# Kernel tuning notes

Measured on AMD Instinct MI355X. Metric: run time of the kernel, lower is better.

Reference implementation:

```python
import jax, jax.numpy as jnp
import numpy as np

N = 100000
E = 1600000
IN_C = 256
HID = 256
OUT_C = 32
K = 2          # APPNP K = max(1, num_layers)
ALPHA = 0.1


def setup_inputs() -> dict:
    key = jax.random.key(0)
    ks = jax.random.split(key, 8)
    x = jax.random.normal(ks[0], (N, IN_C), dtype=jnp.float32)
    edge_index = jax.random.randint(ks[1], (2, E), 0, N, dtype=jnp.int64)
    s_in = 1.0 / np.sqrt(IN_C)
    s_h = 1.0 / np.sqrt(HID)
    W_in = jax.random.uniform(ks[2], (IN_C, HID), jnp.float32, -s_in, s_in)
    b_in = jax.random.uniform(ks[3], (HID,), jnp.float32, -s_in, s_in)
    W_h = jax.random.uniform(ks[4], (HID, HID), jnp.float32, -s_h, s_h)
    b_h = jax.random.uniform(ks[5], (HID,), jnp.float32, -s_h, s_h)
    W_out = jax.random.uniform(ks[6], (HID, OUT_C), jnp.float32, -s_h, s_h)
    b_out = jax.random.uniform(ks[7], (OUT_C,), jnp.float32, -s_h, s_h)
    return {"x": x, "edge_index": edge_index, "W_in": W_in, "b_in": b_in,
            "W_h": W_h, "b_h": b_h, "W_out": W_out, "b_out": b_out}


def _appnp(h0, src, dst):
    # gcn_norm with added self-loops: deg over destinations, sym normalization
    loops = jnp.arange(N, dtype=src.dtype)
    src_f = jnp.concatenate([src, loops])  # [E+N]
    dst_f = jnp.concatenate([dst, loops])
    deg = jax.ops.segment_sum(jnp.ones_like(dst_f, dtype=h0.dtype), dst_f,
                              num_segments=N)
    dinv = jnp.where(deg > 0, jax.lax.rsqrt(jnp.maximum(deg, 1e-12)), 0.0)
    norm = (dinv[src_f] * dinv[dst_f])[:, None]  # [E+N, 1]
    h = h0
    for _ in range(K):
        agg = jax.ops.segment_sum(h[src_f] * norm, dst_f, num_segments=N)
        h = (1.0 - ALPHA) * agg + ALPHA * h0
    return h


def reference(x, edge_index, W_in, b_in, W_h, b_h, W_out, b_out):
    # MLP encoder (dropout inactive in eval mode)
    h = jax.nn.relu(x @ W_in + b_in)
    h = jax.nn.relu(h @ W_h + b_h)
    h = h @ W_out + b_out  # [N, OUT_C]
    return _appnp(h, edge_index[0], edge_index[1])
```

## Files before the change

kernel.cpp:

```cpp
#include <hip/hip_runtime.h>

#define NN 100000
#define NE 1600000
#define NT64 1563

#define BSH 7
#define BNODES 128
#define NBUCK 782
#define NBUCKP 784
#define CAP 2560
#define ECH 8192
#define NCHK 196
#define WFRAG_BLKS 272

typedef _Float16 half8v __attribute__((ext_vector_type(8)));
typedef _Float16 half4v __attribute__((ext_vector_type(4)));
typedef float f32x4 __attribute__((ext_vector_type(4)));


__device__ __forceinline__ void wfrag_one(const float* __restrict__ W,
                                          _Float16* __restrict__ Wf, int idx, int N) {
    int j = idx & 7;
    int l = (idx >> 3) & 63;
    int f = idx >> 9;
    int nt = f % (N / 16);
    int kt = f / (N / 16);
    int k = kt * 32 + (l >> 4) * 8 + j;
    int c = nt * 16 + (l & 15);
    Wf[idx] = (_Float16)W[k * N + c];
}


__global__ __launch_bounds__(512) void k_count_wfrag(const int* __restrict__ dst,
                                                     int* __restrict__ histT,
                                                     const float* __restrict__ W1,
                                                     const float* __restrict__ W2,
                                                     const float* __restrict__ W3,
                                                     _Float16* __restrict__ Wf1,
                                                     _Float16* __restrict__ Wf2,
                                                     _Float16* __restrict__ Wf3) {
    const int t = threadIdx.x;
    if (blockIdx.x >= NCHK) {
        int idx = (blockIdx.x - NCHK) * 512 + t;
        if (idx < 65536) wfrag_one(W1, Wf1, idx, 256);
        else if (idx < 131072) wfrag_one(W2, Wf2, idx - 65536, 256);
        else if (idx < 139264) wfrag_one(W3, Wf3, idx - 131072, 32);
        return;
    }
    __shared__ int h[NBUCKP];
    const int blk = blockIdx.x;
    for (int b = t; b < NBUCKP; b += 512) h[b] = 0;
    __syncthreads();
    const int ebase = blk * ECH + t * 16;
#pragma unroll
    for (int q = 0; q < 4; q++) {
        int e = ebase + q * 4;
        if (e + 4 <= NE) {
            int4 d4 = *reinterpret_cast<const int4*>(dst + e);
            atomicAdd(&h[d4.x >> BSH], 1);
            atomicAdd(&h[d4.y >> BSH], 1);
            atomicAdd(&h[d4.z >> BSH], 1);
            atomicAdd(&h[d4.w >> BSH], 1);
        } else {
            for (int p = e; p < NE; p++) atomicAdd(&h[dst[p] >> BSH], 1);
            break;
        }
    }
    __syncthreads();
    for (int b = t; b < NBUCK; b += 512) histT[(long long)b * NCHK + blk] = h[b];
}


__global__ __launch_bounds__(256) void k_scanb(int* __restrict__ histT,
                                               int* __restrict__ cntb) {
    __shared__ int s[256];
    const int b = blockIdx.x, t = threadIdx.x;
    int* row = histT + (long long)b * NCHK;
    int v = (t < NCHK) ? row[t] : 0;
    s[t] = v;
    __syncthreads();
    for (int off = 1; off < 256; off <<= 1) {
        int u = (t >= off) ? s[t - off] : 0;
        __syncthreads();
        s[t] += u;
        __syncthreads();
    }
    if (t < NCHK) row[t] = s[t] - v;
    if (t == 255) cntb[b] = s[255];
}


__global__ __launch_bounds__(512) void k_part(const int* __restrict__ src,
                                              const int* __restrict__ dst,
                                              const int* __restrict__ histT,
                                              int* __restrict__ data) {
    __shared__ int curs[NBUCKP];
    const int t = threadIdx.x, blk = blockIdx.x;
    for (int b = t; b < NBUCKP; b += 512)
        curs[b] = b * CAP + ((b < NBUCK) ? histT[(long long)b * NCHK + blk] : 0);
    __syncthreads();
    const int ebase = blk * ECH + t * 16;
#pragma unroll
    for (int q = 0; q < 4; q++) {
        int e = ebase + q * 4;
        if (e + 4 <= NE) {
            int4 d4 = *reinterpret_cast<const int4*>(dst + e);
            int4 s4 = *reinterpret_cast<const int4*>(src + e);
            int p0 = atomicAdd(&curs[d4.x >> BSH], 1);
            data[p0] = (s4.x << BSH) | (d4.x & (BNODES - 1));
            int p1 = atomicAdd(&curs[d4.y >> BSH], 1);
            data[p1] = (s4.y << BSH) | (d4.y & (BNODES - 1));
            int p2 = atomicAdd(&curs[d4.z >> BSH], 1);
            data[p2] = (s4.z << BSH) | (d4.z & (BNODES - 1));
            int p3 = atomicAdd(&curs[d4.w >> BSH], 1);
            data[p3] = (s4.w << BSH) | (d4.w & (BNODES - 1));
        } else {
            for (int p = e; p < NE; p++) {
                int d = dst[p], sv = src[p];
                int pos = atomicAdd(&curs[d >> BSH], 1);
                data[pos] = (sv << BSH) | (d & (BNODES - 1));
            }
            break;
        }
    }
}


__global__ __launch_bounds__(256) void k_sortb(const int* __restrict__ data,
                                               const int* __restrict__ cntb,
                                               int* __restrict__ col,
                                               int* __restrict__ begp,
                                               int* __restrict__ endp,
                                               float* __restrict__ dinv) {
    __shared__ int hist[BNODES];
    __shared__ int scn[BNODES];
    __shared__ int curs[BNODES];
    const int b = blockIdx.x, t = threadIdx.x;
    if (t < BNODES) hist[t] = 0;
    __syncthreads();
    const int cnt = cntb[b];
    const int* wp = data + b * CAP;
    for (int e = t; e < cnt; e += 256) atomicAdd(&hist[wp[e] & (BNODES - 1)], 1);
    __syncthreads();
    if (t < BNODES) scn[t] = hist[t];
    __syncthreads();
    for (int off = 1; off < BNODES; off <<= 1) {
        int v = (t < BNODES && t >= off) ? scn[t - off] : 0;
        __syncthreads();
        if (t < BNODES) scn[t] += v;
        __syncthreads();
    }
    if (t < BNODES) {
        int beg = scn[t] - hist[t];
        curs[t] = beg;
        int node = (b << BSH) + t;
        if (node < NN) {
            begp[node] = b * CAP + beg;
            endp[node] = b * CAP + scn[t];
            dinv[node] = rsqrtf((float)(hist[t] + 1));
        }
    }
    __syncthreads();
    for (int e = t; e < cnt; e += 256) {
        int w = wp[e];
        int p = atomicAdd(&curs[w & (BNODES - 1)], 1);
        col[b * CAP + p] = w >> BSH;
    }
}


__global__ __launch_bounds__(512) void k_mlp(const float* __restrict__ x,
                                             const _Float16* __restrict__ Wf1,
                                             const _Float16* __restrict__ Wf2,
                                             const _Float16* __restrict__ Wf3,
                                             const float* __restrict__ b1,
                                             const float* __restrict__ b2,
                                             const float* __restrict__ b3,
                                             const float* __restrict__ dinv,
                                             _Float16* __restrict__ h0f,
                                             _Float16* __restrict__ hs0) {
    __shared__ char buf[64 * 512];
    const int t = threadIdx.x;
    const int lane = t & 63;
    const int G = lane >> 4;
    const int w = t >> 6;
    const int T = blockIdx.x;
    const long long row0 = (long long)T * 64;

    const half8v* W1f = reinterpret_cast<const half8v*>(Wf1);
    const half8v* W2f = reinterpret_cast<const half8v*>(Wf2);
    float bv1[2], bv2[2];
#pragma unroll
    for (int n2 = 0; n2 < 2; n2++) {
        bv1[n2] = b1[w * 32 + n2 * 16 + (lane & 15)];
        bv2[n2] = b2[w * 32 + n2 * 16 + (lane & 15)];
    }

    {
        const float4* A4 = reinterpret_cast<const float4*>(x + row0 * 256);
        float4 v[8];
#pragma unroll
        for (int q = 0; q < 8; q++) {
            int i = t + q * 512;
            int r = i >> 6;
            v[q] = make_float4(0.f, 0.f, 0.f, 0.f);
            if (row0 + r < NN) v[q] = A4[i];
        }
        __builtin_amdgcn_sched_barrier(0);
#pragma unroll
        for (int q = 0; q < 8; q++) {
            int i = t + q * 512;
            int r = i >> 6, c4 = i & 63;
            half4v hv;
            hv[0] = (_Float16)v[q].x; hv[1] = (_Float16)v[q].y;
            hv[2] = (_Float16)v[q].z; hv[3] = (_Float16)v[q].w;
            int bo = (r * 512 + c4 * 8) ^ ((r & 7) << 4);
            *reinterpret_cast<half4v*>(buf + bo) = hv;
        }
    }
    __syncthreads();

    f32x4 acc[4][2];

#pragma unroll
    for (int mt = 0; mt < 4; mt++)
#pragma unroll
        for (int n2 = 0; n2 < 2; n2++) acc[mt][n2] = (f32x4)0.f;
#pragma unroll
    for (int kt = 0; kt < 8; kt++) {
        half8v a[4], bfr[2];
#pragma unroll
        for (int n2 = 0; n2 < 2; n2++)
            bfr[n2] = W1f[(kt * 16 + 2 * w + n2) * 64 + lane];
#pragma unroll
        for (int mt = 0; mt < 4; mt++) {
            int row = mt * 16 + (lane & 15);
            int bo = (row * 512 + kt * 64 + (G << 4)) ^ ((row & 7) << 4);
            a[mt] = *reinterpret_cast<const half8v*>(buf + bo);
        }
#pragma unroll
        for (int mt = 0; mt < 4; mt++)
#pragma unroll
            for (int n2 = 0; n2 < 2; n2++)
                acc[mt][n2] = __builtin_amdgcn_mfma_f32_16x16x32_f16(a[mt], bfr[n2], acc[mt][n2], 0, 0, 0);
    }
    __syncthreads();

#pragma unroll
    for (int mt = 0; mt < 4; mt++)
#pragma unroll
        for (int n2 = 0; n2 < 2; n2++) {
            int colc = w * 32 + n2 * 16 + (lane & 15);
            float bb = bv1[n2];
#pragma unroll
            for (int r = 0; r < 4; r++) {
                int row = mt * 16 + G * 4 + r;
                float v = fmaxf(acc[mt][n2][r] + bb, 0.f);
                int bo = (row * 512 + colc * 2) ^ ((row & 7) << 4);
                *reinterpret_cast<_Float16*>(buf + bo) = (_Float16)v;
            }
        }
    __syncthreads();

#pragma unroll
    for (int mt = 0; mt < 4; mt++)
#pragma unroll
        for (int n2 = 0; n2 < 2; n2++) acc[mt][n2] = (f32x4)0.f;
#pragma unroll
    for (int kt = 0; kt < 8; kt++) {
        half8v a[4], bfr[2];
#pragma unroll
        for (int n2 = 0; n2 < 2; n2++)
            bfr[n2] = W2f[(kt * 16 + 2 * w + n2) * 64 + lane];
#pragma unroll
        for (int mt = 0; mt < 4; mt++) {
            int row = mt * 16 + (lane & 15);
            int bo = (row * 512 + kt * 64 + (G << 4)) ^ ((row & 7) << 4);
            a[mt] = *reinterpret_cast<const half8v*>(buf + bo);
        }
#pragma unroll
        for (int mt = 0; mt < 4; mt++)
#pragma unroll
            for (int n2 = 0; n2 < 2; n2++)
                acc[mt][n2] = __builtin_amdgcn_mfma_f32_16x16x32_f16(a[mt], bfr[n2], acc[mt][n2], 0, 0, 0);
    }
    __syncthreads();

#pragma unroll
    for (int mt = 0; mt < 4; mt++)
#pragma unroll
        for (int n2 = 0; n2 < 2; n2++) {
            int colc = w * 32 + n2 * 16 + (lane & 15);
            float bb = bv2[n2];
#pragma unroll
            for (int r = 0; r < 4; r++) {
                int row = mt * 16 + G * 4 + r;
                float v = fmaxf(acc[mt][n2][r] + bb, 0.f);
                int bo = (row * 512 + colc * 2) ^ ((row & 7) << 4);
                *reinterpret_cast<_Float16*>(buf + bo) = (_Float16)v;
            }
        }
    __syncthreads();

    {
        const half8v* W3f = reinterpret_cast<const half8v*>(Wf3);
        const int mt3 = w >> 1, ct3 = w & 1;
        const float bb3 = b3[ct3 * 16 + (lane & 15)];
        f32x4 a3 = (f32x4)0.f;
#pragma unroll
        for (int kt = 0; kt < 8; kt++) {
            int row = mt3 * 16 + (lane & 15);
            int bo = (row * 512 + kt * 64 + (G << 4)) ^ ((row & 7) << 4);
            half8v a = *reinterpret_cast<const half8v*>(buf + bo);
            half8v b = W3f[(kt * 2 + ct3) * 64 + lane];
            a3 = __builtin_amdgcn_mfma_f32_16x16x32_f16(a, b, a3, 0, 0, 0);
        }
        int colc = ct3 * 16 + (lane & 15);
#pragma unroll
        for (int r = 0; r < 4; r++) {
            long long row = row0 + mt3 * 16 + G * 4 + r;
            if (row < NN) {
                float v = a3[r] + bb3;
                h0f[row * 32 + colc] = (_Float16)v;
                hs0[row * 32 + colc] = (_Float16)(dinv[row] * v);
            }
        }
    }
}


template<bool FINAL>
__global__ __launch_bounds__(256) void k_appnp(const int* __restrict__ begp,
                                               const int* __restrict__ endp,
                                               const int* __restrict__ col,
                                               const float* __restrict__ dinv,
                                               const _Float16* __restrict__ hs,
                                               const _Float16* __restrict__ h0f,
                                               void* __restrict__ outp) {
    int node = blockIdx.x * 4 + (threadIdx.x >> 6);
    if (node >= NN) return;
    const int lane = threadIdx.x & 63;
    const int slot = lane >> 2;
    const int cg = lane & 3;

    const int beg = begp[node];
    const int end = endp[node];
    const float dd = dinv[node];
    const half8v selfv = *reinterpret_cast<const half8v*>(hs + (size_t)node * 32 + cg * 8);
    const half8v h0v = *reinterpret_cast<const half8v*>(h0f + (size_t)node * 32 + cg * 8);

    float acc[8];
#pragma unroll
    for (int j = 0; j < 8; j++) acc[j] = 0.f;

    for (int e = beg + slot; e < end; e += 16) {
        int s = col[e];
        half8v v = *reinterpret_cast<const half8v*>(hs + (size_t)s * 32 + cg * 8);
#pragma unroll
        for (int j = 0; j < 8; j++) acc[j] += (float)v[j];
    }

#pragma unroll
    for (int off = 4; off < 64; off <<= 1) {
#pragma unroll
        for (int j = 0; j < 8; j++) acc[j] += __shfl_xor(acc[j], off, 64);
    }

    if (slot == 0) {
        float o[8];
#pragma unroll
        for (int j = 0; j < 8; j++)
            o[j] = 0.9f * dd * (acc[j] + (float)selfv[j]) + 0.1f * (float)h0v[j];
        size_t off = (size_t)node * 32 + cg * 8;
        if (FINAL) {
            float4 v0 = make_float4(o[0], o[1], o[2], o[3]);
            float4 v1 = make_float4(o[4], o[5], o[6], o[7]);
            float4* op = reinterpret_cast<float4*>((float*)outp + off);
            op[0] = v0; op[1] = v1;
        } else {
            half8v hv;
#pragma unroll
            for (int j = 0; j < 8; j++) hv[j] = (_Float16)(dd * o[j]);
            *reinterpret_cast<half8v*>((_Float16*)outp + off) = hv;
        }
    }
}


extern "C" void kernel_launch(void* const* d_in, const int* in_sizes, int n_in,
                              void* d_out, int out_size, void* d_ws, size_t ws_size,
                              hipStream_t stream) {
    const float* x     = (const float*)d_in[0];
    const int*   ei    = (const int*)d_in[1];
    const float* W_in  = (const float*)d_in[2];
    const float* b_in  = (const float*)d_in[3];
    const float* W_h   = (const float*)d_in[4];
    const float* b_h   = (const float*)d_in[5];
    const float* W_out = (const float*)d_in[6];
    const float* b_out = (const float*)d_in[7];
    float* out = (float*)d_out;

    const int* srcv = ei;
    const int* dstv = ei + NE;

    char* ws = (char*)d_ws;
    _Float16* h0f  = (_Float16*)ws;
    _Float16* hs0  = h0f + (size_t)NN * 32;
    _Float16* hs1  = hs0 + (size_t)NN * 32;
    float* dinv    = (float*)(hs1 + (size_t)NN * 32);
    _Float16* Wf_in  = (_Float16*)(dinv + NN);
    _Float16* Wf_h   = Wf_in + 256 * 256;
    _Float16* Wf_out = Wf_h + 256 * 256;
    int* histT = (int*)(Wf_out + 256 * 32);
    int* cntb  = histT + (size_t)NBUCK * NCHK;
    int* data  = cntb + NBUCKP;
    int* col   = data + (size_t)NBUCKP * CAP;
    int* begp  = col + (size_t)NBUCKP * CAP;
    int* endp  = begp + NN;

    k_count_wfrag<<<NCHK + WFRAG_BLKS, 512, 0, stream>>>(dstv, histT,
                                                         W_in, W_h, W_out,
                                                         Wf_in, Wf_h, Wf_out);
    k_scanb<<<NBUCK, 256, 0, stream>>>(histT, cntb);

    k_part<<<NCHK, 512, 0, stream>>>(srcv, dstv, histT, data);

    k_sortb<<<NBUCK, 256, 0, stream>>>(data, cntb, col, begp, endp, dinv);

    k_mlp<<<NT64, 512, 0, stream>>>(x, Wf_in, Wf_h, Wf_out, b_in, b_h, b_out,
                                    dinv, h0f, hs0);

    k_appnp<false><<<(NN + 3) / 4, 256, 0, stream>>>(begp, endp, col, dinv, hs0, h0f, hs1);
    k_appnp<true ><<<(NN + 3) / 4, 256, 0, stream>>>(begp, endp, col, dinv, hs1, h0f, out);
}
```

Before: 170.8 us.

## Merge edge partition with MLP launch and defer dinv scaling to sort kernel

Removes the MLP's dependence on dinv so the edge partition blocks and the MLP blocks can share one launch and run concurrently. Degree computation moves to a small separate kernel, and the dinv-scaled copy hs0 is now produced by extra blocks appended to the bucket sort kernel. The goal is to hide the latency-bound partition and sort phases behind the compute-heavy MLP. The cost is one additional launch (k_deg), a second pass over the bucketed data to count degrees, and an extra read and write of h0f to build hs0.

```diff
diff --git a/kernel.cpp b/kernel.cpp
--- a/kernel.cpp
+++ b/kernel.cpp
@@ -3,6 +3,7 @@
 #define NN 100000
 #define NE 1600000
 #define NT64 1563
+#define SCALE_BLKS 1563
 
 #define BSH 7
 #define BNODES 128
@@ -90,101 +91,59 @@
 }
 
 
-__global__ __launch_bounds__(512) void k_part(const int* __restrict__ src,
-                                              const int* __restrict__ dst,
-                                              const int* __restrict__ histT,
-                                              int* __restrict__ data) {
-    __shared__ int curs[NBUCKP];
-    const int t = threadIdx.x, blk = blockIdx.x;
-    for (int b = t; b < NBUCKP; b += 512)
-        curs[b] = b * CAP + ((b < NBUCK) ? histT[(long long)b * NCHK + blk] : 0);
-    __syncthreads();
-    const int ebase = blk * ECH + t * 16;
-#pragma unroll
-    for (int q = 0; q < 4; q++) {
-        int e = ebase + q * 4;
-        if (e + 4 <= NE) {
-            int4 d4 = *reinterpret_cast<const int4*>(dst + e);
-            int4 s4 = *reinterpret_cast<const int4*>(src + e);
-            int p0 = atomicAdd(&curs[d4.x >> BSH], 1);
-            data[p0] = (s4.x << BSH) | (d4.x & (BNODES - 1));
-            int p1 = atomicAdd(&curs[d4.y >> BSH], 1);
-            data[p1] = (s4.y << BSH) | (d4.y & (BNODES - 1));
-            int p2 = atomicAdd(&curs[d4.z >> BSH], 1);
-            data[p2] = (s4.z << BSH) | (d4.z & (BNODES - 1));
-            int p3 = atomicAdd(&curs[d4.w >> BSH], 1);
-            data[p3] = (s4.w << BSH) | (d4.w & (BNODES - 1));
-        } else {
-            for (int p = e; p < NE; p++) {
-                int d = dst[p], sv = src[p];
-                int pos = atomicAdd(&curs[d >> BSH], 1);
-                data[pos] = (sv << BSH) | (d & (BNODES - 1));
+__global__ __launch_bounds__(512) void k_part_mlp(const int* __restrict__ src,
+                                                  const int* __restrict__ dst,
+                                                  const int* __restrict__ histT,
+                                                  int* __restrict__ data,
+                                                  const float* __restrict__ x,
+                                                  const _Float16* __restrict__ Wf1,
+                                                  const _Float16* __restrict__ Wf2,
+                                                  const _Float16* __restrict__ Wf3,
+                                                  const float* __restrict__ b1,
+                                                  const float* __restrict__ b2,
+                                                  const float* __restrict__ b3,
+                                                  _Float16* __restrict__ h0f) {
+    __shared__ char smem[32768];
+    const int t = threadIdx.x;
+
+    if (blockIdx.x < NCHK) {
+        int* curs = (int*)smem;
+        const int blk = blockIdx.x;
+        for (int b = t; b < NBUCKP; b += 512)
+            curs[b] = b * CAP + ((b < NBUCK) ? histT[(long long)b * NCHK + blk] : 0);
+        __syncthreads();
+        const int ebase = blk * ECH + t * 16;
+#pragma unroll
+        for (int q = 0; q < 4; q++) {
+            int e = ebase + q * 4;
+            if (e + 4 <= NE) {
+                int4 d4 = *reinterpret_cast<const int4*>(dst + e);
+                int4 s4 = *reinterpret_cast<const int4*>(src + e);
+                int p0 = atomicAdd(&curs[d4.x >> BSH], 1);
+                data[p0] = (s4.x << BSH) | (d4.x & (BNODES - 1));
+                int p1 = atomicAdd(&curs[d4.y >> BSH], 1);
+                data[p1] = (s4.y << BSH) | (d4.y & (BNODES - 1));
+                int p2 = atomicAdd(&curs[d4.z >> BSH], 1);
+                data[p2] = (s4.z << BSH) | (d4.z & (BNODES - 1));
+                int p3 = atomicAdd(&curs[d4.w >> BSH], 1);
+                data[p3] = (s4.w << BSH) | (d4.w & (BNODES - 1));
+            } else {
+                for (int p = e; p < NE; p++) {
+                    int d = dst[p], sv = src[p];
+                    int pos = atomicAdd(&curs[d >> BSH], 1);
+                    data[pos] = (sv << BSH) | (d & (BNODES - 1));
+                }
+                break;
             }
-            break;
-        }
-    }
-}
-
-
-__global__ __launch_bounds__(256) void k_sortb(const int* __restrict__ data,
-                                               const int* __restrict__ cntb,
-                                               int* __restrict__ col,
-                                               int* __restrict__ begp,
-                                               int* __restrict__ endp,
-                                               float* __restrict__ dinv) {
-    __shared__ int hist[BNODES];
-    __shared__ int scn[BNODES];
-    __shared__ int curs[BNODES];
-    const int b = blockIdx.x, t = threadIdx.x;
-    if (t < BNODES) hist[t] = 0;
-    __syncthreads();
-    const int cnt = cntb[b];
-    const int* wp = data + b * CAP;
-    for (int e = t; e < cnt; e += 256) atomicAdd(&hist[wp[e] & (BNODES - 1)], 1);
-    __syncthreads();
-    if (t < BNODES) scn[t] = hist[t];
-    __syncthreads();
-    for (int off = 1; off < BNODES; off <<= 1) {
-        int v = (t < BNODES && t >= off) ? scn[t - off] : 0;
-        __syncthreads();
-        if (t < BNODES) scn[t] += v;
-        __syncthreads();
-    }
-    if (t < BNODES) {
-        int beg = scn[t] - hist[t];
-        curs[t] = beg;
-        int node = (b << BSH) + t;
-        if (node < NN) {
-            begp[node] = b * CAP + beg;
-            endp[node] = b * CAP + scn[t];
-            dinv[node] = rsqrtf((float)(hist[t] + 1));
-        }
-    }
-    __syncthreads();
-    for (int e = t; e < cnt; e += 256) {
-        int w = wp[e];
-        int p = atomicAdd(&curs[w & (BNODES - 1)], 1);
-        col[b * CAP + p] = w >> BSH;
-    }
-}
-
-
-__global__ __launch_bounds__(512) void k_mlp(const float* __restrict__ x,
-                                             const _Float16* __restrict__ Wf1,
-                                             const _Float16* __restrict__ Wf2,
-                                             const _Float16* __restrict__ Wf3,
-                                             const float* __restrict__ b1,
-                                             const float* __restrict__ b2,
-                                             const float* __restrict__ b3,
-                                             const float* __restrict__ dinv,
-                                             _Float16* __restrict__ h0f,
-                                             _Float16* __restrict__ hs0) {
-    __shared__ char buf[64 * 512];
-    const int t = threadIdx.x;
+        }
+        return;
+    }
+
+    char* buf = smem;
     const int lane = t & 63;
     const int G = lane >> 4;
     const int w = t >> 6;
-    const int T = blockIdx.x;
+    const int T = blockIdx.x - NCHK;
     const long long row0 = (long long)T * 64;
 
     const half8v* W1f = reinterpret_cast<const half8v*>(Wf1);
@@ -319,12 +278,82 @@
 #pragma unroll
         for (int r = 0; r < 4; r++) {
             long long row = row0 + mt3 * 16 + G * 4 + r;
-            if (row < NN) {
-                float v = a3[r] + bb3;
-                h0f[row * 32 + colc] = (_Float16)v;
-                hs0[row * 32 + colc] = (_Float16)(dinv[row] * v);
-            }
-        }
+            if (row < NN) h0f[row * 32 + colc] = (_Float16)(a3[r] + bb3);
+        }
+    }
+}
+
+
+__global__ __launch_bounds__(256) void k_deg(const int* __restrict__ data,
+                                             const int* __restrict__ cntb,
+                                             float* __restrict__ dinv) {
+    __shared__ int c[BNODES];
+    const int b = blockIdx.x, t = threadIdx.x;
+    if (t < BNODES) c[t] = 0;
+    __syncthreads();
+    const int cnt = cntb[b];
+    const int* wp = data + b * CAP;
+    for (int e = t; e < cnt; e += 256) atomicAdd(&c[wp[e] & (BNODES - 1)], 1);
+    __syncthreads();
+    int node = (b << BSH) + t;
+    if (t < BNODES && node < NN) dinv[node] = rsqrtf((float)(c[t] + 1));
+}
+
+
+__global__ __launch_bounds__(256) void k_sortb_scale(const int* __restrict__ data,
+                                                     const int* __restrict__ cntb,
+                                                     int* __restrict__ col,
+                                                     int* __restrict__ begp,
+                                                     int* __restrict__ endp,
+                                                     const float* __restrict__ dinv,
+                                                     const _Float16* __restrict__ h0f,
+                                                     _Float16* __restrict__ hs0) {
+    const int t = threadIdx.x;
+    if (blockIdx.x >= NBUCK) {
+        int idx = (blockIdx.x - NBUCK) * 256 + t;
+        if (idx < NN * 4) {
+            int node = idx >> 2;
+            float dd = dinv[node];
+            half8v v = *reinterpret_cast<const half8v*>(h0f + (size_t)idx * 8);
+            half8v o;
+#pragma unroll
+            for (int j = 0; j < 8; j++) o[j] = (_Float16)(dd * (float)v[j]);
+            *reinterpret_cast<half8v*>(hs0 + (size_t)idx * 8) = o;
+        }
+        return;
+    }
+    __shared__ int hist[BNODES];
+    __shared__ int scn[BNODES];
+    __shared__ int curs[BNODES];
+    const int b = blockIdx.x;
+    if (t < BNODES) hist[t] = 0;
+    __syncthreads();
+    const int cnt = cntb[b];
+    const int* wp = data + b * CAP;
+    for (int e = t; e < cnt; e += 256) atomicAdd(&hist[wp[e] & (BNODES - 1)], 1);
+    __syncthreads();
+    if (t < BNODES) scn[t] = hist[t];
+    __syncthreads();
+    for (int off = 1; off < BNODES; off <<= 1) {
+        int v = (t < BNODES && t >= off) ? scn[t - off] : 0;
+        __syncthreads();
+        if (t < BNODES) scn[t] += v;
+        __syncthreads();
+    }
+    if (t < BNODES) {
+        int beg = scn[t] - hist[t];
+        curs[t] = beg;
+        int node = (b << BSH) + t;
+        if (node < NN) {
+            begp[node] = b * CAP + beg;
+            endp[node] = b * CAP + scn[t];
+        }
+    }
+    __syncthreads();
+    for (int e = t; e < cnt; e += 256) {
+        int w = wp[e];
+        int p = atomicAdd(&curs[w & (BNODES - 1)], 1);
+        col[b * CAP + p] = w >> BSH;
     }
 }
 
@@ -423,12 +452,14 @@
                                                          Wf_in, Wf_h, Wf_out);
     k_scanb<<<NBUCK, 256, 0, stream>>>(histT, cntb);
 
-    k_part<<<NCHK, 512, 0, stream>>>(srcv, dstv, histT, data);
-
-    k_sortb<<<NBUCK, 256, 0, stream>>>(data, cntb, col, begp, endp, dinv);
-
-    k_mlp<<<NT64, 512, 0, stream>>>(x, Wf_in, Wf_h, Wf_out, b_in, b_h, b_out,
-                                    dinv, h0f, hs0);
+    k_part_mlp<<<NCHK + NT64, 512, 0, stream>>>(srcv, dstv, histT, data,
+                                                x, Wf_in, Wf_h, Wf_out,
+                                                b_in, b_h, b_out, h0f);
+
+    k_deg<<<NBUCK, 256, 0, stream>>>(data, cntb, dinv);
+
+    k_sortb_scale<<<NBUCK + SCALE_BLKS, 256, 0, stream>>>(data, cntb, col, begp, endp,
+                                                          dinv, h0f, hs0);
 
     k_appnp<false><<<(NN + 3) / 4, 256, 0, stream>>>(begp, endp, col, dinv, hs0, h0f, hs1);
     k_appnp<true ><<<(NN + 3) / 4, 256, 0, stream>>>(begp, endp, col, dinv, hs1, h0f, out);
```

Measured after the change: 155.0 us, median of 3. 9.2% less time.

## Merge edge partition with MLP kernel and drop dinv-prescaled h0 buffer

Applied to the files above, without the earlier changes.

Folds the edge-partition pass and the MLP encoder into one launch, split by block index, so the memory-bound scatter and the MFMA-heavy MLP can run concurrently on the GPU. The MLP no longer depends on dinv, and k_sortb now runs after it. The first propagation step reads unscaled h0 and multiplies each gathered neighbour by dinv[s] on the fly, which removes the hs0 buffer and its write. The cost is an extra per-edge dinv gather in the first APPNP pass.

```diff
diff --git a/kernel.cpp b/kernel.cpp
--- a/kernel.cpp
+++ b/kernel.cpp
@@ -90,37 +90,194 @@
 }
 
 
-__global__ __launch_bounds__(512) void k_part(const int* __restrict__ src,
-                                              const int* __restrict__ dst,
-                                              const int* __restrict__ histT,
-                                              int* __restrict__ data) {
-    __shared__ int curs[NBUCKP];
-    const int t = threadIdx.x, blk = blockIdx.x;
-    for (int b = t; b < NBUCKP; b += 512)
-        curs[b] = b * CAP + ((b < NBUCK) ? histT[(long long)b * NCHK + blk] : 0);
-    __syncthreads();
-    const int ebase = blk * ECH + t * 16;
-#pragma unroll
-    for (int q = 0; q < 4; q++) {
-        int e = ebase + q * 4;
-        if (e + 4 <= NE) {
-            int4 d4 = *reinterpret_cast<const int4*>(dst + e);
-            int4 s4 = *reinterpret_cast<const int4*>(src + e);
-            int p0 = atomicAdd(&curs[d4.x >> BSH], 1);
-            data[p0] = (s4.x << BSH) | (d4.x & (BNODES - 1));
-            int p1 = atomicAdd(&curs[d4.y >> BSH], 1);
-            data[p1] = (s4.y << BSH) | (d4.y & (BNODES - 1));
-            int p2 = atomicAdd(&curs[d4.z >> BSH], 1);
-            data[p2] = (s4.z << BSH) | (d4.z & (BNODES - 1));
-            int p3 = atomicAdd(&curs[d4.w >> BSH], 1);
-            data[p3] = (s4.w << BSH) | (d4.w & (BNODES - 1));
-        } else {
-            for (int p = e; p < NE; p++) {
-                int d = dst[p], sv = src[p];
-                int pos = atomicAdd(&curs[d >> BSH], 1);
-                data[pos] = (sv << BSH) | (d & (BNODES - 1));
+__global__ __launch_bounds__(512) void k_part_mlp(const int* __restrict__ src,
+                                                  const int* __restrict__ dst,
+                                                  const int* __restrict__ histT,
+                                                  int* __restrict__ data,
+                                                  const float* __restrict__ x,
+                                                  const _Float16* __restrict__ Wf1,
+                                                  const _Float16* __restrict__ Wf2,
+                                                  const _Float16* __restrict__ Wf3,
+                                                  const float* __restrict__ b1,
+                                                  const float* __restrict__ b2,
+                                                  const float* __restrict__ b3,
+                                                  _Float16* __restrict__ h0f) {
+    __shared__ char smem[32768];
+    const int t = threadIdx.x;
+
+    if (blockIdx.x < NCHK) {
+        int* curs = (int*)smem;
+        const int blk = blockIdx.x;
+        for (int b = t; b < NBUCKP; b += 512)
+            curs[b] = b * CAP + ((b < NBUCK) ? histT[(long long)b * NCHK + blk] : 0);
+        __syncthreads();
+        const int ebase = blk * ECH + t * 16;
+#pragma unroll
+        for (int q = 0; q < 4; q++) {
+            int e = ebase + q * 4;
+            if (e + 4 <= NE) {
+                int4 d4 = *reinterpret_cast<const int4*>(dst + e);
+                int4 s4 = *reinterpret_cast<const int4*>(src + e);
+                int p0 = atomicAdd(&curs[d4.x >> BSH], 1);
+                data[p0] = (s4.x << BSH) | (d4.x & (BNODES - 1));
+                int p1 = atomicAdd(&curs[d4.y >> BSH], 1);
+                data[p1] = (s4.y << BSH) | (d4.y & (BNODES - 1));
+                int p2 = atomicAdd(&curs[d4.z >> BSH], 1);
+                data[p2] = (s4.z << BSH) | (d4.z & (BNODES - 1));
+                int p3 = atomicAdd(&curs[d4.w >> BSH], 1);
+                data[p3] = (s4.w << BSH) | (d4.w & (BNODES - 1));
+            } else {
+                for (int p = e; p < NE; p++) {
+                    int d = dst[p], sv = src[p];
+                    int pos = atomicAdd(&curs[d >> BSH], 1);
+                    data[pos] = (sv << BSH) | (d & (BNODES - 1));
+                }
+                break;
             }
-            break;
+        }
+        return;
+    }
+
+    char* buf = smem;
+    const int lane = t & 63;
+    const int G = lane >> 4;
+    const int w = t >> 6;
+    const int T = blockIdx.x - NCHK;
+    const long long row0 = (long long)T * 64;
+
+    const half8v* W1f = reinterpret_cast<const half8v*>(Wf1);
+    const half8v* W2f = reinterpret_cast<const half8v*>(Wf2);
+    float bv1[2], bv2[2];
+#pragma unroll
+    for (int n2 = 0; n2 < 2; n2++) {
+        bv1[n2] = b1[w * 32 + n2 * 16 + (lane & 15)];
+        bv2[n2] = b2[w * 32 + n2 * 16 + (lane & 15)];
+    }
+
+    {
+        const float4* A4 = reinterpret_cast<const float4*>(x + row0 * 256);
+        float4 v[8];
+#pragma unroll
+        for (int q = 0; q < 8; q++) {
+            int i = t + q * 512;
+            int r = i >> 6;
+            v[q] = make_float4(0.f, 0.f, 0.f, 0.f);
+            if (row0 + r < NN) v[q] = A4[i];
+        }
+        __builtin_amdgcn_sched_barrier(0);
+#pragma unroll
+        for (int q = 0; q < 8; q++) {
+            int i = t + q * 512;
+            int r = i >> 6, c4 = i & 63;
+            half4v hv;
+            hv[0] = (_Float16)v[q].x; hv[1] = (_Float16)v[q].y;
+            hv[2] = (_Float16)v[q].z; hv[3] = (_Float16)v[q].w;
+            int bo = (r * 512 + c4 * 8) ^ ((r & 7) << 4);
+            *reinterpret_cast<half4v*>(buf + bo) = hv;
+        }
+    }
+    __syncthreads();
+
+    f32x4 acc[4][2];
+
+#pragma unroll
+    for (int mt = 0; mt < 4; mt++)
+#pragma unroll
+        for (int n2 = 0; n2 < 2; n2++) acc[mt][n2] = (f32x4)0.f;
+#pragma unroll
+    for (int kt = 0; kt < 8; kt++) {
+        half8v a[4], bfr[2];
+#pragma unroll
+        for (int n2 = 0; n2 < 2; n2++)
+            bfr[n2] = W1f[(kt * 16 + 2 * w + n2) * 64 + lane];
+#pragma unroll
+        for (int mt = 0; mt < 4; mt++) {
+            int row = mt * 16 + (lane & 15);
+            int bo = (row * 512 + kt * 64 + (G << 4)) ^ ((row & 7) << 4);
+            a[mt] = *reinterpret_cast<const half8v*>(buf + bo);
+        }
+#pragma unroll
+        for (int mt = 0; mt < 4; mt++)
+#pragma unroll
+            for (int n2 = 0; n2 < 2; n2++)
+                acc[mt][n2] = __builtin_amdgcn_mfma_f32_16x16x32_f16(a[mt], bfr[n2], acc[mt][n2], 0, 0, 0);
+    }
+    __syncthreads();
+
+#pragma unroll
+    for (int mt = 0; mt < 4; mt++)
+#pragma unroll
+        for (int n2 = 0; n2 < 2; n2++) {
+            int colc = w * 32 + n2 * 16 + (lane & 15);
+            float bb = bv1[n2];
+#pragma unroll
+            for (int r = 0; r < 4; r++) {
+                int row = mt * 16 + G * 4 + r;
+                float v = fmaxf(acc[mt][n2][r] + bb, 0.f);
+                int bo = (row * 512 + colc * 2) ^ ((row & 7) << 4);
+                *reinterpret_cast<_Float16*>(buf + bo) = (_Float16)v;
+            }
+        }
+    __syncthreads();
+
+#pragma unroll
+    for (int mt = 0; mt < 4; mt++)
+#pragma unroll
+        for (int n2 = 0; n2 < 2; n2++) acc[mt][n2] = (f32x4)0.f;
+#pragma unroll
+    for (int kt = 0; kt < 8; kt++) {
+        half8v a[4], bfr[2];
+#pragma unroll
+        for (int n2 = 0; n2 < 2; n2++)
+            bfr[n2] = W2f[(kt * 16 + 2 * w + n2) * 64 + lane];
+#pragma unroll
+        for (int mt = 0; mt < 4; mt++) {
+            int row = mt * 16 + (lane & 15);
+            int bo = (row * 512 + kt * 64 + (G << 4)) ^ ((row & 7) << 4);
+            a[mt] = *reinterpret_cast<const half8v*>(buf + bo);
+        }
+#pragma unroll
+        for (int mt = 0; mt < 4; mt++)
+#pragma unroll
+            for (int n2 = 0; n2 < 2; n2++)
+                acc[mt][n2] = __builtin_amdgcn_mfma_f32_16x16x32_f16(a[mt], bfr[n2], acc[mt][n2], 0, 0, 0);
+    }
+    __syncthreads();
+
+#pragma unroll
+    for (int mt = 0; mt < 4; mt++)
+#pragma unroll
+        for (int n2 = 0; n2 < 2; n2++) {
+            int colc = w * 32 + n2 * 16 + (lane & 15);
+            float bb = bv2[n2];
+#pragma unroll
+            for (int r = 0; r < 4; r++) {
+                int row = mt * 16 + G * 4 + r;
+                float v = fmaxf(acc[mt][n2][r] + bb, 0.f);
+                int bo = (row * 512 + colc * 2) ^ ((row & 7) << 4);
+                *reinterpret_cast<_Float16*>(buf + bo) = (_Float16)v;
+            }
+        }
+    __syncthreads();
+
+    {
+        const half8v* W3f = reinterpret_cast<const half8v*>(Wf3);
+        const int mt3 = w >> 1, ct3 = w & 1;
+        const float bb3 = b3[ct3 * 16 + (lane & 15)];
+        f32x4 a3 = (f32x4)0.f;
+#pragma unroll
+        for (int kt = 0; kt < 8; kt++) {
+            int row = mt3 * 16 + (lane & 15);
+            int bo = (row * 512 + kt * 64 + (G << 4)) ^ ((row & 7) << 4);
+            half8v a = *reinterpret_cast<const half8v*>(buf + bo);
+            half8v b = W3f[(kt * 2 + ct3) * 64 + lane];
+            a3 = __builtin_amdgcn_mfma_f32_16x16x32_f16(a, b, a3, 0, 0, 0);
+        }
+        int colc = ct3 * 16 + (lane & 15);
+#pragma unroll
+        for (int r = 0; r < 4; r++) {
+            long long row = row0 + mt3 * 16 + G * 4 + r;
+            if (row < NN) h0f[row * 32 + colc] = (_Float16)(a3[r] + bb3);
         }
     }
 }
@@ -165,166 +322,6 @@
         int w = wp[e];
         int p = atomicAdd(&curs[w & (BNODES - 1)], 1);
         col[b * CAP + p] = w >> BSH;
-    }
-}
-
-
-__global__ __launch_bounds__(512) void k_mlp(const float* __restrict__ x,
-                                             const _Float16* __restrict__ Wf1,
-                                             const _Float16* __restrict__ Wf2,
-                                             const _Float16* __restrict__ Wf3,
-                                             const float* __restrict__ b1,
-                                             const float* __restrict__ b2,
-                                             const float* __restrict__ b3,
-                                             const float* __restrict__ dinv,
-                                             _Float16* __restrict__ h0f,
-                                             _Float16* __restrict__ hs0) {
-    __shared__ char buf[64 * 512];
-    const int t = threadIdx.x;
-    const int lane = t & 63;
-    const int G = lane >> 4;
-    const int w = t >> 6;
-    const int T = blockIdx.x;
-    const long long row0 = (long long)T * 64;
-
-    const half8v* W1f = reinterpret_cast<const half8v*>(Wf1);
-    const half8v* W2f = reinterpret_cast<const half8v*>(Wf2);
-    float bv1[2], bv2[2];
-#pragma unroll
-    for (int n2 = 0; n2 < 2; n2++) {
-        bv1[n2] = b1[w * 32 + n2 * 16 + (lane & 15)];
-        bv2[n2] = b2[w * 32 + n2 * 16 + (lane & 15)];
-    }
-
-    {
-        const float4* A4 = reinterpret_cast<const float4*>(x + row0 * 256);
-        float4 v[8];
-#pragma unroll
-        for (int q = 0; q < 8; q++) {
-            int i = t + q * 512;
-            int r = i >> 6;
-            v[q] = make_float4(0.f, 0.f, 0.f, 0.f);
-            if (row0 + r < NN) v[q] = A4[i];
-        }
-        __builtin_amdgcn_sched_barrier(0);
-#pragma unroll
-        for (int q = 0; q < 8; q++) {
-            int i = t + q * 512;
-            int r = i >> 6, c4 = i & 63;
-            half4v hv;
-            hv[0] = (_Float16)v[q].x; hv[1] = (_Float16)v[q].y;
-            hv[2] = (_Float16)v[q].z; hv[3] = (_Float16)v[q].w;
-            int bo = (r * 512 + c4 * 8) ^ ((r & 7) << 4);
-            *reinterpret_cast<half4v*>(buf + bo) = hv;
-        }
-    }
-    __syncthreads();
-
-    f32x4 acc[4][2];
-
-#pragma unroll
-    for (int mt = 0; mt < 4; mt++)
-#pragma unroll
-        for (int n2 = 0; n2 < 2; n2++) acc[mt][n2] = (f32x4)0.f;
-#pragma unroll
-    for (int kt = 0; kt < 8; kt++) {
-        half8v a[4], bfr[2];
-#pragma unroll
-        for (int n2 = 0; n2 < 2; n2++)
-            bfr[n2] = W1f[(kt * 16 + 2 * w + n2) * 64 + lane];
-#pragma unroll
-        for (int mt = 0; mt < 4; mt++) {
-            int row = mt * 16 + (lane & 15);
-            int bo = (row * 512 + kt * 64 + (G << 4)) ^ ((row & 7) << 4);
-            a[mt] = *reinterpret_cast<const half8v*>(buf + bo);
-        }
-#pragma unroll
-        for (int mt = 0; mt < 4; mt++)
-#pragma unroll
-            for (int n2 = 0; n2 < 2; n2++)
-                acc[mt][n2] = __builtin_amdgcn_mfma_f32_16x16x32_f16(a[mt], bfr[n2], acc[mt][n2], 0, 0, 0);
-    }
-    __syncthreads();
-
-#pragma unroll
-    for (int mt = 0; mt < 4; mt++)
-#pragma unroll
-        for (int n2 = 0; n2 < 2; n2++) {
-            int colc = w * 32 + n2 * 16 + (lane & 15);
-            float bb = bv1[n2];
-#pragma unroll
-            for (int r = 0; r < 4; r++) {
-                int row = mt * 16 + G * 4 + r;
-                float v = fmaxf(acc[mt][n2][r] + bb, 0.f);
-                int bo = (row * 512 + colc * 2) ^ ((row & 7) << 4);
-                *reinterpret_cast<_Float16*>(buf + bo) = (_Float16)v;
-            }
-        }
-    __syncthreads();
-
-#pragma unroll
-    for (int mt = 0; mt < 4; mt++)
-#pragma unroll
-        for (int n2 = 0; n2 < 2; n2++) acc[mt][n2] = (f32x4)0.f;
-#pragma unroll
-    for (int kt = 0; kt < 8; kt++) {
-        half8v a[4], bfr[2];
-#pragma unroll
-        for (int n2 = 0; n2 < 2; n2++)
-            bfr[n2] = W2f[(kt * 16 + 2 * w + n2) * 64 + lane];
-#pragma unroll
-        for (int mt = 0; mt < 4; mt++) {
-            int row = mt * 16 + (lane & 15);
-            int bo = (row * 512 + kt * 64 + (G << 4)) ^ ((row & 7) << 4);
-            a[mt] = *reinterpret_cast<const half8v*>(buf + bo);
-        }
-#pragma unroll
-        for (int mt = 0; mt < 4; mt++)
-#pragma unroll
-            for (int n2 = 0; n2 < 2; n2++)
-                acc[mt][n2] = __builtin_amdgcn_mfma_f32_16x16x32_f16(a[mt], bfr[n2], acc[mt][n2], 0, 0, 0);
-    }
-    __syncthreads();
-
-#pragma unroll
-    for (int mt = 0; mt < 4; mt++)
-#pragma unroll
-        for (int n2 = 0; n2 < 2; n2++) {
-            int colc = w * 32 + n2 * 16 + (lane & 15);
-            float bb = bv2[n2];
-#pragma unroll
-            for (int r = 0; r < 4; r++) {
-                int row = mt * 16 + G * 4 + r;
-                float v = fmaxf(acc[mt][n2][r] + bb, 0.f);
-                int bo = (row * 512 + colc * 2) ^ ((row & 7) << 4);
-                *reinterpret_cast<_Float16*>(buf + bo) = (_Float16)v;
-            }
-        }
-    __syncthreads();
-
-    {
-        const half8v* W3f = reinterpret_cast<const half8v*>(Wf3);
-        const int mt3 = w >> 1, ct3 = w & 1;
-        const float bb3 = b3[ct3 * 16 + (lane & 15)];
-        f32x4 a3 = (f32x4)0.f;
-#pragma unroll
-        for (int kt = 0; kt < 8; kt++) {
-            int row = mt3 * 16 + (lane & 15);
-            int bo = (row * 512 + kt * 64 + (G << 4)) ^ ((row & 7) << 4);
-            half8v a = *reinterpret_cast<const half8v*>(buf + bo);
-            half8v b = W3f[(kt * 2 + ct3) * 64 + lane];
-            a3 = __builtin_amdgcn_mfma_f32_16x16x32_f16(a, b, a3, 0, 0, 0);
-        }
-        int colc = ct3 * 16 + (lane & 15);
-#pragma unroll
-        for (int r = 0; r < 4; r++) {
-            long long row = row0 + mt3 * 16 + G * 4 + r;
-            if (row < NN) {
-                float v = a3[r] + bb3;
-                h0f[row * 32 + colc] = (_Float16)v;
-                hs0[row * 32 + colc] = (_Float16)(dinv[row] * v);
-            }
-        }
     }
 }
 
@@ -347,7 +344,6 @@
     const int end = endp[node];
     const float dd = dinv[node];
     const half8v selfv = *reinterpret_cast<const half8v*>(hs + (size_t)node * 32 + cg * 8);
-    const half8v h0v = *reinterpret_cast<const half8v*>(h0f + (size_t)node * 32 + cg * 8);
 
     float acc[8];
 #pragma unroll
@@ -356,8 +352,10 @@
     for (int e = beg + slot; e < end; e += 16) {
         int s = col[e];
         half8v v = *reinterpret_cast<const half8v*>(hs + (size_t)s * 32 + cg * 8);
-#pragma unroll
-        for (int j = 0; j < 8; j++) acc[j] += (float)v[j];
+        float sc = 1.f;
+        if (!FINAL) sc = dinv[s];
+#pragma unroll
+        for (int j = 0; j < 8; j++) acc[j] += sc * (float)v[j];
     }
 
 #pragma unroll
@@ -367,12 +365,13 @@
     }
 
     if (slot == 0) {
-        float o[8];
-#pragma unroll
-        for (int j = 0; j < 8; j++)
-            o[j] = 0.9f * dd * (acc[j] + (float)selfv[j]) + 0.1f * (float)h0v[j];
         size_t off = (size_t)node * 32 + cg * 8;
         if (FINAL) {
+            const half8v h0v = *reinterpret_cast<const half8v*>(h0f + off);
+            float o[8];
+#pragma unroll
+            for (int j = 0; j < 8; j++)
+                o[j] = 0.9f * dd * (acc[j] + (float)selfv[j]) + 0.1f * (float)h0v[j];
             float4 v0 = make_float4(o[0], o[1], o[2], o[3]);
             float4 v1 = make_float4(o[4], o[5], o[6], o[7]);
             float4* op = reinterpret_cast<float4*>((float*)outp + off);
@@ -380,7 +379,11 @@
         } else {
             half8v hv;
 #pragma unroll
-            for (int j = 0; j < 8; j++) hv[j] = (_Float16)(dd * o[j]);
+            for (int j = 0; j < 8; j++) {
+                float sv = (float)selfv[j];
+                float hnew = 0.9f * dd * (acc[j] + dd * sv) + 0.1f * sv;
+                hv[j] = (_Float16)(dd * hnew);
+            }
             *reinterpret_cast<half8v*>((_Float16*)outp + off) = hv;
         }
     }
@@ -405,8 +408,7 @@
 
     char* ws = (char*)d_ws;
     _Float16* h0f  = (_Float16*)ws;
-    _Float16* hs0  = h0f + (size_t)NN * 32;
-    _Float16* hs1  = hs0 + (size_t)NN * 32;
+    _Float16* hs1  = h0f + (size_t)NN * 32;
     float* dinv    = (float*)(hs1 + (size_t)NN * 32);
     _Float16* Wf_in  = (_Float16*)(dinv + NN);
     _Float16* Wf_h   = Wf_in + 256 * 256;
@@ -423,13 +425,12 @@
                                                          Wf_in, Wf_h, Wf_out);
     k_scanb<<<NBUCK, 256, 0, stream>>>(histT, cntb);
 
-    k_part<<<NCHK, 512, 0, stream>>>(srcv, dstv, histT, data);
+    k_part_mlp<<<NCHK + NT64, 512, 0, stream>>>(srcv, dstv, histT, data,
+                                                x, Wf_in, Wf_h, Wf_out,
+                                                b_in, b_h, b_out, h0f);
 
     k_sortb<<<NBUCK, 256, 0, stream>>>(data, cntb, col, begp, endp, dinv);
 
-    k_mlp<<<NT64, 512, 0, stream>>>(x, Wf_in, Wf_h, Wf_out, b_in, b_h, b_out,
-                                    dinv, h0f, hs0);
-
-    k_appnp<false><<<(NN + 3) / 4, 256, 0, stream>>>(begp, endp, col, dinv, hs0, h0f, hs1);
+    k_appnp<false><<<(NN + 3) / 4, 256, 0, stream>>>(begp, endp, col, dinv, h0f, h0f, hs1);
     k_appnp<true ><<<(NN + 3) / 4, 256, 0, stream>>>(begp, endp, col, dinv, hs1, h0f, out);
 }
```

Result: faster. 153.2 us, median of 2 (-10.3%).
